# Kernel tuning notes

Hardware: AMD Instinct MI355X
Metric: run time of the kernel (lower is better)

The kernel has to match this reference:

```python
import jax, jax.numpy as jnp
import numpy as np

N_NODES = 100000
N_EDGES = 1600000
NODE_DIM = 32
EDGE_DIM = 16
OUT_DIM = 32


def setup_inputs() -> dict:
    key = jax.random.key(0)
    ks = jax.random.split(key, 8)
    D = NODE_DIM + EDGE_DIM  # 48
    return {
        "y": jax.random.normal(ks[0], (N_NODES, NODE_DIM), dtype=jnp.float32),
        "ex": jax.random.normal(ks[1], (N_EDGES, EDGE_DIM), dtype=jnp.float32),
        "W1": jax.random.normal(ks[2], (D, D), dtype=jnp.float32) / np.sqrt(D),
        "b1": jax.random.normal(ks[3], (D,), dtype=jnp.float32) * 0.01,
        "W2": jax.random.normal(ks[4], (OUT_DIM, D), dtype=jnp.float32) / np.sqrt(D),
        "b2": jax.random.normal(ks[5], (OUT_DIM,), dtype=jnp.float32) * 0.01,
        "src": jax.random.randint(ks[6], (N_EDGES,), 0, N_NODES, dtype=jnp.int32),
        "dst": jax.random.randint(ks[7], (N_EDGES,), 0, N_NODES, dtype=jnp.int32),
    }


def reference(y, ex, W1, b1, W2, b2, src, dst):
    n_nodes = y.shape[0]
    # per-edge message: ReLU(Linear(concat(y[src], e_x)))  -> [E, node_dim+edge_dim]
    feat = jnp.concatenate([y[src], ex], axis=1)
    m = jax.nn.relu(feat @ W1.T + b1)
    # mean scatter-reduce onto destination nodes (0 for isolated nodes, DGL semantics)
    s = jax.ops.segment_sum(m, dst, num_segments=n_nodes)
    cnt = jax.ops.segment_sum(jnp.ones((m.shape[0],), m.dtype), dst, num_segments=n_nodes)
    z = jnp.where(cnt[:, None] > 0, s / jnp.maximum(cnt, 1.0)[:, None], 0.0)
    # node update: ReLU(Linear(z)) -> [N, out_dim]
    h = jax.nn.relu(z @ W2.T + b2)
    return h
```

## Files before the change

kernel.cpp:

```cpp
#include <hip/hip_runtime.h>

#define NODE_DIM 32
#define EDGE_DIM 16
#define DD 48
#define OUT_DIM 32
#define MAXDEG 64
#define NXCD 8
#define NPW 16

typedef _Float16 f16x8 __attribute__((ext_vector_type(8)));
typedef float f32x4 __attribute__((ext_vector_type(4)));

__global__ __launch_bounds__(256)
void prep_kernel(int* __restrict__ cursor, int ZB, int NC,
                 const float* __restrict__ y, _Float16* __restrict__ yh, int CBy,
                 const float* __restrict__ ex, _Float16* __restrict__ exh,
                 int N, int E) {
    int b = blockIdx.x;
    if (b < ZB) {
        int i = (b * 256 + threadIdx.x) * 4;
        if (i < NC) *reinterpret_cast<int4*>(cursor + i) = make_int4(0, 0, 0, 0);
        return;
    }
    b -= ZB;
    if (b < CBy) {
        size_t i = ((size_t)b * 256 + threadIdx.x) * 8;
        if (i < (size_t)N * NODE_DIM) {
            const float4* s0 = reinterpret_cast<const float4*>(y + i);
            const float4 a = s0[0], c = s0[1];
            f16x8 h = {(_Float16)a.x, (_Float16)a.y, (_Float16)a.z, (_Float16)a.w,
                       (_Float16)c.x, (_Float16)c.y, (_Float16)c.z, (_Float16)c.w};
            *reinterpret_cast<f16x8*>(yh + i) = h;
        }
        return;
    }
    b -= CBy;
    size_t i = ((size_t)b * 256 + threadIdx.x) * 8;
    if (i < (size_t)E * EDGE_DIM) {
        const float4* s0 = reinterpret_cast<const float4*>(ex + i);
        const float4 a = s0[0], c = s0[1];
        f16x8 h = {(_Float16)a.x, (_Float16)a.y, (_Float16)a.z, (_Float16)a.w,
                   (_Float16)c.x, (_Float16)c.y, (_Float16)c.z, (_Float16)c.w};
        *reinterpret_cast<f16x8*>(exh + i) = h;
    }
}

__global__ __launch_bounds__(256)
void scatter_kernel(const int* __restrict__ dst, const int* __restrict__ src,
                    int* __restrict__ cursor, int2* __restrict__ meta,
                    int E, int NP) {
    const int xcd = blockIdx.x & (NXCD - 1);
    const int c   = blockIdx.x >> 3;
    const int base = c * 2048 + threadIdx.x * 8;
    if (base >= E) return;

    int dv[8], sv[8];
    if (base + 8 <= E) {
        *reinterpret_cast<int4*>(dv)     = *reinterpret_cast<const int4*>(dst + base);
        *reinterpret_cast<int4*>(dv + 4) = *reinterpret_cast<const int4*>(dst + base + 4);
        *reinterpret_cast<int4*>(sv)     = *reinterpret_cast<const int4*>(src + base);
        *reinterpret_cast<int4*>(sv + 4) = *reinterpret_cast<const int4*>(src + base + 4);
    } else {
#pragma unroll
        for (int i = 0; i < 8; ++i) {
            dv[i] = (base + i < E) ? dst[base + i] : -1;
            sv[i] = (base + i < E) ? src[base + i] : 0;
        }
    }
#pragma unroll
    for (int i = 0; i < 8; ++i) {
        const int d = dv[i];
        if (d >= 0 && (d & (NXCD - 1)) == xcd && base + i < E) {
            int pos = atomicAdd(&cursor[xcd * NP + (d >> 3)], 1);
            if (pos < MAXDEG)
                meta[(size_t)d * MAXDEG + pos] = make_int2(base + i, sv[i]);
        }
    }
}

__global__ __launch_bounds__(256)
void fused_kernel(const _Float16* __restrict__ yh, const _Float16* __restrict__ exh,
                  const float* __restrict__ W1, const float* __restrict__ b1,
                  const float* __restrict__ W2, const float* __restrict__ b2,
                  const int* __restrict__ cursor, const int2* __restrict__ meta,
                  float* __restrict__ out, int N, int NP) {
    __shared__ int2 mlds[4][NPW][MAXDEG];
    __shared__ _Float16 zl[4][NPW][64];

    const int wave = threadIdx.x >> 6;
    const int lane = threadIdx.x & 63;
    const int col = lane & 15;
    const int kg  = lane >> 4;

    f16x8 Blo[3], Bhi[3];
#pragma unroll
    for (int t = 0; t < 3; ++t) {
        const float* wr = W1 + (size_t)(t * 16 + col) * DD;
#pragma unroll
        for (int j = 0; j < 8; ++j) {
            Blo[t][j] = (_Float16)wr[kg * 8 + j];
            Bhi[t][j] = (_Float16)0.f;
        }
        if (kg < 2) {
#pragma unroll
            for (int j = 0; j < 8; ++j)
                Bhi[t][j] = (_Float16)wr[NODE_DIM + kg * 8 + j];
        }
        if (kg == 3) Bhi[t][7] = (_Float16)b1[t * 16 + col];
    }

    f16x8 Wf[2][2];
#pragma unroll
    for (int t = 0; t < 2; ++t) {
#pragma unroll
        for (int c = 0; c < 2; ++c) {
            f16x8 v;
#pragma unroll
            for (int j = 0; j < 8; ++j) {
                const int k = c * 32 + kg * 8 + j;
                float w = 0.f;
                if (k < DD)       w = W2[(size_t)(t * 16 + col) * DD + k];
                else if (k == DD) w = b2[t * 16 + col];
                v[j] = (_Float16)w;
            }
            Wf[t][c] = v;
        }
    }

    const int nb0 = (blockIdx.x * 4 + wave) * NPW;

    int dgv = 0;
    if (lane < NPW) {
        const int n = nb0 + lane;
        if (n < N) dgv = cursor[(n & (NXCD - 1)) * NP + (n >> 3)];
    }

#pragma unroll
    for (int ni = 0; ni < NPW; ++ni) {
        const int cnt_i = min(__shfl(dgv, ni), MAXDEG);
        const int n = nb0 + ni;
        mlds[wave][ni][lane] = (lane < cnt_i && n < N)
                                   ? meta[(size_t)n * MAXDEG + lane]
                                   : make_int2(0, 0);
    }
    __builtin_amdgcn_wave_barrier();

    for (int ni = 0; ni < NPW; ++ni) {
        const int n = nb0 + ni;
        const int dg = __shfl(dgv, ni);
        const int cnt = min(dg, MAXDEG);

        float pacc0 = 0.f, pacc1 = 0.f, pacc2 = 0.f;
        const int ngroups = (cnt + 15) >> 4;

        for (int g = 0; g < ngroups; ++g) {
            const bool valid = (g * 16 + col) < cnt;
            const int2 md = mlds[wave][ni][g * 16 + col];
            const int eid = md.x, sv = md.y;

            f16x8 alo = *reinterpret_cast<const f16x8*>(
                yh + (size_t)sv * NODE_DIM + kg * 8);

            f16x8 ahi;
            if (kg < 2) {
                ahi = *reinterpret_cast<const f16x8*>(
                    exh + (size_t)eid * EDGE_DIM + kg * 8);
            } else {
#pragma unroll
                for (int j = 0; j < 8; ++j) ahi[j] = (_Float16)0.f;
                if (kg == 3) ahi[7] = (_Float16)1.f;
            }

            if (!valid) {
#pragma unroll
                for (int j = 0; j < 8; ++j) { alo[j] = (_Float16)0.f; ahi[j] = (_Float16)0.f; }
            }

#pragma unroll
            for (int t = 0; t < 3; ++t) {
                f32x4 c = {0.f, 0.f, 0.f, 0.f};
                c = __builtin_amdgcn_mfma_f32_16x16x32_f16(alo, Blo[t], c, 0, 0, 0);
                c = __builtin_amdgcn_mfma_f32_16x16x32_f16(ahi, Bhi[t], c, 0, 0, 0);
#pragma unroll
                for (int r = 0; r < 4; ++r) {
                    const float v = fmaxf(c[r], 0.f);
                    if (t == 0) pacc0 += v;
                    else if (t == 1) pacc1 += v;
                    else pacc2 += v;
                }
            }
        }

        pacc0 += __shfl_xor(pacc0, 16); pacc0 += __shfl_xor(pacc0, 32);
        pacc1 += __shfl_xor(pacc1, 16); pacc1 += __shfl_xor(pacc1, 32);
        pacc2 += __shfl_xor(pacc2, 16); pacc2 += __shfl_xor(pacc2, 32);

        if (n < N) {
            const float inv = (dg > 0) ? 1.f / (float)dg : 0.f;
            if (lane < 16) {
                zl[wave][ni][lane]      = (_Float16)(pacc0 * inv);
                zl[wave][ni][lane + 16] = (_Float16)(pacc1 * inv);
                zl[wave][ni][lane + 32] = (_Float16)(pacc2 * inv);
            }
            if (lane < 8) {
                const unsigned int v = (lane == 0) ? 0x00003C00u : 0u;
                *reinterpret_cast<unsigned int*>(&zl[wave][ni][48 + lane * 2]) = v;
            }
        } else if (lane < 32) {
            *reinterpret_cast<unsigned int*>(&zl[wave][ni][lane * 2]) = 0u;
        }
        __builtin_amdgcn_wave_barrier();
    }

    __builtin_amdgcn_wave_barrier();
    const _Float16* zr = &zl[wave][col][0];
    const f16x8 A0 = *reinterpret_cast<const f16x8*>(zr + kg * 8);
    const f16x8 A1 = *reinterpret_cast<const f16x8*>(zr + 32 + kg * 8);

#pragma unroll
    for (int t = 0; t < 2; ++t) {
        f32x4 h = {0.f, 0.f, 0.f, 0.f};
        h = __builtin_amdgcn_mfma_f32_16x16x32_f16(A0, Wf[t][0], h, 0, 0, 0);
        h = __builtin_amdgcn_mfma_f32_16x16x32_f16(A1, Wf[t][1], h, 0, 0, 0);
#pragma unroll
        for (int r = 0; r < 4; ++r) {
            const int node = nb0 + kg * 4 + r;
            if (node < N)
                out[(size_t)node * OUT_DIM + t * 16 + col] = fmaxf(h[r], 0.f);
        }
    }
}

extern "C" void kernel_launch(void* const* d_in, const int* in_sizes, int n_in,
                              void* d_out, int out_size, void* d_ws, size_t ws_size,
                              hipStream_t stream) {
    const float* y  = (const float*)d_in[0];
    const float* ex = (const float*)d_in[1];
    const float* W1 = (const float*)d_in[2];
    const float* b1 = (const float*)d_in[3];
    const float* W2 = (const float*)d_in[4];
    const float* b2 = (const float*)d_in[5];
    const int* src  = (const int*)d_in[6];
    const int* dst  = (const int*)d_in[7];

    const int N = in_sizes[0] / NODE_DIM;
    const int E = in_sizes[6];
    const int NP = (N + NXCD - 1) / NXCD;
    const int NC = ((NXCD * NP + 3) / 4) * 4;

    int* cursor = (int*)d_ws;
    size_t off  = ((size_t)NC * sizeof(int) + 255) & ~(size_t)255;
    int2* meta  = (int2*)((char*)d_ws + off);
    _Float16* yh = (_Float16*)((char*)meta + (size_t)N * MAXDEG * sizeof(int2));
    _Float16* exh = (_Float16*)((char*)yh + (size_t)N * NODE_DIM * sizeof(_Float16));

    const int ZB  = (NC / 4 + 255) / 256;
    const int CBy = (N * NODE_DIM / 8 + 255) / 256;
    const int CBe = (E * EDGE_DIM / 8 + 255) / 256;

    prep_kernel<<<ZB + CBy + CBe, 256, 0, stream>>>(cursor, ZB, NC,
                                                    y, yh, CBy, ex, exh, N, E);

    const int K = (E + 2047) / 2048;
    scatter_kernel<<<K * NXCD, 256, 0, stream>>>(dst, src, cursor, meta, E, NP);

    const int NB = (N + NPW * 4 - 1) / (NPW * 4);
    fused_kernel<<<NB, 256, 0, stream>>>(yh, exh, W1, b1, W2, b2,
                                         cursor, meta, (float*)d_out, N, NP);
}
```

Baseline: 185.7 us.

## Merge scatter into prep kernel, memset cursor, halve per-wave metadata LDS

The edge-bucketing scatter is folded into the fp16 conversion kernel as extra leading blocks, so bucketing and conversion run concurrently in one launch. Cursor zeroing moves to a hipMemsetAsync ahead of that launch. In the fused kernel the per-wave edge-metadata staging buffer is cut from 16 to 8 nodes and refilled halfway through, which halves its LDS footprint and may raise occupancy, and the per-node wave barrier is dropped. The cost is a memset launch plus a mid-loop restaging step in the fused kernel.

```diff
diff --git a/kernel.cpp b/kernel.cpp
--- a/kernel.cpp
+++ b/kernel.cpp
@@ -12,17 +12,44 @@
 typedef float f32x4 __attribute__((ext_vector_type(4)));
 
 __global__ __launch_bounds__(256)
-void prep_kernel(int* __restrict__ cursor, int ZB, int NC,
-                 const float* __restrict__ y, _Float16* __restrict__ yh, int CBy,
-                 const float* __restrict__ ex, _Float16* __restrict__ exh,
-                 int N, int E) {
+void prep_scatter_kernel(const int* __restrict__ dst, const int* __restrict__ src,
+                         int* __restrict__ cursor, int2* __restrict__ meta,
+                         int E, int SBt, int NP,
+                         const float* __restrict__ y, _Float16* __restrict__ yh,
+                         int CBy, const float* __restrict__ ex,
+                         _Float16* __restrict__ exh, int N) {
     int b = blockIdx.x;
-    if (b < ZB) {
-        int i = (b * 256 + threadIdx.x) * 4;
-        if (i < NC) *reinterpret_cast<int4*>(cursor + i) = make_int4(0, 0, 0, 0);
+    if (b < SBt) {
+        const int xcd = b & (NXCD - 1);
+        const int c   = b >> 3;
+        const int base = c * 2048 + threadIdx.x * 8;
+        if (base >= E) return;
+
+        int dv[8], sv[8];
+        if (base + 8 <= E) {
+            *reinterpret_cast<int4*>(dv)     = *reinterpret_cast<const int4*>(dst + base);
+            *reinterpret_cast<int4*>(dv + 4) = *reinterpret_cast<const int4*>(dst + base + 4);
+            *reinterpret_cast<int4*>(sv)     = *reinterpret_cast<const int4*>(src + base);
+            *reinterpret_cast<int4*>(sv + 4) = *reinterpret_cast<const int4*>(src + base + 4);
+        } else {
+#pragma unroll
+            for (int i = 0; i < 8; ++i) {
+                dv[i] = (base + i < E) ? dst[base + i] : -1;
+                sv[i] = (base + i < E) ? src[base + i] : 0;
+            }
+        }
+#pragma unroll
+        for (int i = 0; i < 8; ++i) {
+            const int d = dv[i];
+            if (d >= 0 && (d & (NXCD - 1)) == xcd && base + i < E) {
+                int pos = atomicAdd(&cursor[xcd * NP + (d >> 3)], 1);
+                if (pos < MAXDEG)
+                    meta[(size_t)d * MAXDEG + pos] = make_int2(base + i, sv[i]);
+            }
+        }
         return;
     }
-    b -= ZB;
+    b -= SBt;
     if (b < CBy) {
         size_t i = ((size_t)b * 256 + threadIdx.x) * 8;
         if (i < (size_t)N * NODE_DIM) {
@@ -46,45 +73,12 @@
 }
 
 __global__ __launch_bounds__(256)
-void scatter_kernel(const int* __restrict__ dst, const int* __restrict__ src,
-                    int* __restrict__ cursor, int2* __restrict__ meta,
-                    int E, int NP) {
-    const int xcd = blockIdx.x & (NXCD - 1);
-    const int c   = blockIdx.x >> 3;
-    const int base = c * 2048 + threadIdx.x * 8;
-    if (base >= E) return;
-
-    int dv[8], sv[8];
-    if (base + 8 <= E) {
-        *reinterpret_cast<int4*>(dv)     = *reinterpret_cast<const int4*>(dst + base);
-        *reinterpret_cast<int4*>(dv + 4) = *reinterpret_cast<const int4*>(dst + base + 4);
-        *reinterpret_cast<int4*>(sv)     = *reinterpret_cast<const int4*>(src + base);
-        *reinterpret_cast<int4*>(sv + 4) = *reinterpret_cast<const int4*>(src + base + 4);
-    } else {
-#pragma unroll
-        for (int i = 0; i < 8; ++i) {
-            dv[i] = (base + i < E) ? dst[base + i] : -1;
-            sv[i] = (base + i < E) ? src[base + i] : 0;
-        }
-    }
-#pragma unroll
-    for (int i = 0; i < 8; ++i) {
-        const int d = dv[i];
-        if (d >= 0 && (d & (NXCD - 1)) == xcd && base + i < E) {
-            int pos = atomicAdd(&cursor[xcd * NP + (d >> 3)], 1);
-            if (pos < MAXDEG)
-                meta[(size_t)d * MAXDEG + pos] = make_int2(base + i, sv[i]);
-        }
-    }
-}
-
-__global__ __launch_bounds__(256)
 void fused_kernel(const _Float16* __restrict__ yh, const _Float16* __restrict__ exh,
                   const float* __restrict__ W1, const float* __restrict__ b1,
                   const float* __restrict__ W2, const float* __restrict__ b2,
                   const int* __restrict__ cursor, const int2* __restrict__ meta,
                   float* __restrict__ out, int N, int NP) {
-    __shared__ int2 mlds[4][NPW][MAXDEG];
+    __shared__ int2 mlds[4][8][MAXDEG];
     __shared__ _Float16 zl[4][NPW][64];
 
     const int wave = threadIdx.x >> 6;
@@ -135,17 +129,27 @@
         if (n < N) dgv = cursor[(n & (NXCD - 1)) * NP + (n >> 3)];
     }
 
-#pragma unroll
+    auto stage8 = [&](int b0) {
+#pragma unroll
+        for (int k = 0; k < 8; ++k) {
+            const int ni = b0 + k;
+            const int cnt_i = min(__shfl(dgv, ni), MAXDEG);
+            const int n = nb0 + ni;
+            mlds[wave][k][lane] = (lane < cnt_i && n < N)
+                                      ? meta[(size_t)n * MAXDEG + lane]
+                                      : make_int2(0, 0);
+        }
+    };
+    stage8(0);
+    __builtin_amdgcn_wave_barrier();
+
     for (int ni = 0; ni < NPW; ++ni) {
-        const int cnt_i = min(__shfl(dgv, ni), MAXDEG);
-        const int n = nb0 + ni;
-        mlds[wave][ni][lane] = (lane < cnt_i && n < N)
-                                   ? meta[(size_t)n * MAXDEG + lane]
-                                   : make_int2(0, 0);
-    }
-    __builtin_amdgcn_wave_barrier();
-
-    for (int ni = 0; ni < NPW; ++ni) {
+        if (ni == 8) {
+            __builtin_amdgcn_wave_barrier();
+            stage8(8);
+            __builtin_amdgcn_wave_barrier();
+        }
+        const int slot = ni & 7;
         const int n = nb0 + ni;
         const int dg = __shfl(dgv, ni);
         const int cnt = min(dg, MAXDEG);
@@ -155,7 +159,7 @@
 
         for (int g = 0; g < ngroups; ++g) {
             const bool valid = (g * 16 + col) < cnt;
-            const int2 md = mlds[wave][ni][g * 16 + col];
+            const int2 md = mlds[wave][slot][g * 16 + col];
             const int eid = md.x, sv = md.y;
 
             f16x8 alo = *reinterpret_cast<const f16x8*>(
@@ -209,7 +213,6 @@
         } else if (lane < 32) {
             *reinterpret_cast<unsigned int*>(&zl[wave][ni][lane * 2]) = 0u;
         }
-        __builtin_amdgcn_wave_barrier();
     }
 
     __builtin_amdgcn_wave_barrier();
@@ -254,15 +257,14 @@
     _Float16* yh = (_Float16*)((char*)meta + (size_t)N * MAXDEG * sizeof(int2));
     _Float16* exh = (_Float16*)((char*)yh + (size_t)N * NODE_DIM * sizeof(_Float16));
 
-    const int ZB  = (NC / 4 + 255) / 256;
+    const int SBt = ((E + 2047) / 2048) * NXCD;
     const int CBy = (N * NODE_DIM / 8 + 255) / 256;
     const int CBe = (E * EDGE_DIM / 8 + 255) / 256;
 
-    prep_kernel<<<ZB + CBy + CBe, 256, 0, stream>>>(cursor, ZB, NC,
-                                                    y, yh, CBy, ex, exh, N, E);
-
-    const int K = (E + 2047) / 2048;
-    scatter_kernel<<<K * NXCD, 256, 0, stream>>>(dst, src, cursor, meta, E, NP);
+    hipMemsetAsync(cursor, 0, (size_t)NC * sizeof(int), stream);
+
+    prep_scatter_kernel<<<SBt + CBy + CBe, 256, 0, stream>>>(
+        dst, src, cursor, meta, E, SBt, NP, y, yh, CBy, ex, exh, N);
 
     const int NB = (N + NPW * 4 - 1) / (NPW * 4);
     fused_kernel<<<NB, 256, 0, stream>>>(yh, exh, W1, b1, W2, b2,
```

Result: slower. 203.4 us (+9.5%).
